# Kernel tuning notes

Hardware: AMD Instinct MI355X
Metric: run time of the kernel (lower is better)

Reference implementation:

```python
import jax, jax.numpy as jnp
import numpy as np

C64 = jnp.complex64


def _apply_1q(state, G, wire):
    # state: [B,2,2,2,2]; G: [2,2] (shared) or [B,2,2] (per-sample)
    s = jnp.moveaxis(state, wire + 1, -1)
    if G.ndim == 2:
        s = jnp.einsum('ij,b...j->b...i', G, s)
    else:
        s = jnp.einsum('bij,b...j->b...i', G, s)
    return jnp.moveaxis(s, -1, wire + 1)


def _apply_cnot(state, c, t):
    s = jnp.moveaxis(state, (c + 1, t + 1), (-2, -1))
    s = jnp.concatenate([s[..., :1, :], s[..., 1:, ::-1]], axis=-2)
    return jnp.moveaxis(s, (-2, -1), (c + 1, t + 1))


def _rx_batch(theta):
    # theta: [B,4] -> gates [B,4,2,2] (PennyLane AngleEmbedding default = RX)
    c = jnp.cos(theta * 0.5).astype(C64)
    s = (-1j * jnp.sin(theta * 0.5)).astype(C64)
    return jnp.stack([jnp.stack([c, s], -1), jnp.stack([s, c], -1)], -2)


def _ry(theta):
    c = jnp.cos(theta * 0.5).astype(C64)
    s = jnp.sin(theta * 0.5).astype(C64)
    return jnp.stack([jnp.stack([c, -s]), jnp.stack([s, c])])


def _rz(theta):
    t = theta.astype(C64)
    return jnp.diag(jnp.stack([jnp.exp(-0.5j * t), jnp.exp(0.5j * t)]))


def _circuit(features, q_params):
    # features: [B,4] angles, q_params: [8]. Returns <Z_w> per wire: [B,4]
    B = features.shape[0]
    state = jnp.zeros((B, 2, 2, 2, 2), C64).at[:, 0, 0, 0, 0].set(1.0)
    Gx = _rx_batch(features)  # [B,4,2,2]
    for w in range(4):
        state = _apply_1q(state, Gx[:, w], w)
    for w in range(4):
        state = _apply_1q(state, _ry(q_params[w]), w)
    for w in range(3):
        state = _apply_cnot(state, w, w + 1)
    for w in range(4):
        state = _apply_1q(state, _rz(q_params[4 + w]), w)
    probs = state.real ** 2 + state.imag ** 2  # [B,2,2,2,2]
    sign = jnp.array([1.0, -1.0], jnp.float32)
    exps = [jnp.sum(probs * sign.reshape([1] + [2 if a == w else 1 for a in range(4)]),
                    axis=(1, 2, 3, 4)) for w in range(4)]
    return jnp.stack(exps, -1)


def setup_inputs() -> dict:
    key = jax.random.key(0)
    ks = jax.random.split(key, 8)
    B = 65536
    return {
        'x': jax.random.normal(ks[0], (B, 1, 36, 36), jnp.float32),
        'q_params': jax.random.normal(ks[1], (8,), jnp.float32),
        'W1': jax.random.normal(ks[2], (64, 4), jnp.float32) * 0.5,
        'b1': jax.random.normal(ks[3], (64,), jnp.float32) * 0.1,
        'W2': jax.random.normal(ks[4], (4, 64), jnp.float32) * 0.125,
        'b2': jax.random.normal(ks[5], (4,), jnp.float32) * 0.1,
        'gamma': jnp.ones((4,), jnp.float32),
        'beta': jnp.zeros((4,), jnp.float32),
    }


def reference(x, q_params, W1, b1, W2, b2, gamma, beta):
    B = x.shape[0]
    # avg_pool2d(kernel=6, stride=6) on [B,1,36,36] -> [B,1,6,6] -> flatten
    pooled = x.reshape(B, 1, 6, 6, 6, 6).mean(axis=(3, 5)).reshape(B, -1)
    features = pooled[:, :4]
    q_out = _circuit(features, q_params)             # [B,4]
    h = jax.nn.relu(q_out @ W1.T + b1)               # [B,64]
    logits = h @ W2.T + b2                           # [B,4]
    # BatchNorm1d (training mode: batch stats, biased var, eps=1e-5)
    mu = logits.mean(axis=0)
    var = ((logits - mu) ** 2).mean(axis=0)
    return gamma * (logits - mu) / jnp.sqrt(var + 1e-5) + beta
```

## Files before the change

### kernel.cpp

```cpp
#include <hip/hip_runtime.h>
#include <math.h>


__global__ void k_init(float* acc) {
    if (threadIdx.x < 8) acc[threadIdx.x] = 0.0f;
}

__global__ __launch_bounds__(256) void k_main(
    const float* __restrict__ x,
    const float* __restrict__ qp,
    const float* __restrict__ W1,
    const float* __restrict__ b1,
    const float* __restrict__ W2,
    const float* __restrict__ b2,
    float* __restrict__ logits,
    float* __restrict__ acc,
    int B)
{
    __shared__ float sW1[256];
    __shared__ float sW2t[256];
    __shared__ float sb1[64];
    __shared__ float sred[32];

    const int tid = threadIdx.x;
    sW1[tid]  = W1[tid];
    sW2t[tid] = W2[(tid & 3) * 64 + (tid >> 2)];
    if (tid < 64) sb1[tid] = b1[tid];
    __syncthreads();

    const int b = blockIdx.x * 256 + tid;
    float l0 = 0.f, l1 = 0.f, l2 = 0.f, l3 = 0.f;

    if (b < B) {
        const float* xb = x + (size_t)b * 1296;
        float f0 = 0.f, f1 = 0.f, f2 = 0.f, f3 = 0.f;
        #pragma unroll
        for (int r = 0; r < 6; ++r) {
            const float4* row = (const float4*)(xb + r * 36);
            float4 v0 = row[0], v1 = row[1], v2 = row[2];
            float4 v3 = row[3], v4 = row[4], v5 = row[5];
            f0 += v0.x + v0.y + v0.z + v0.w + v1.x + v1.y;
            f1 += v1.z + v1.w + v2.x + v2.y + v2.z + v2.w;
            f2 += v3.x + v3.y + v3.z + v3.w + v4.x + v4.y;
            f3 += v4.z + v4.w + v5.x + v5.y + v5.z + v5.w;
        }
        const float inv36 = 1.0f / 36.0f;
        float z0 = cosf(qp[0]) * cosf(f0 * inv36);
        float z1 = cosf(qp[1]) * cosf(f1 * inv36);
        float z2 = cosf(qp[2]) * cosf(f2 * inv36);
        float z3 = cosf(qp[3]) * cosf(f3 * inv36);
        float q0 = z0;
        float q1 = q0 * z1;
        float q2 = q1 * z2;
        float q3 = q2 * z3;

        l0 = b2[0]; l1 = b2[1]; l2 = b2[2]; l3 = b2[3];
        #pragma unroll 8
        for (int j = 0; j < 64; ++j) {
            float h = sb1[j];
            h = fmaf(sW1[4*j+0], q0, h);
            h = fmaf(sW1[4*j+1], q1, h);
            h = fmaf(sW1[4*j+2], q2, h);
            h = fmaxf(fmaf(sW1[4*j+3], q3, h), 0.0f);
            l0 = fmaf(sW2t[4*j+0], h, l0);
            l1 = fmaf(sW2t[4*j+1], h, l1);
            l2 = fmaf(sW2t[4*j+2], h, l2);
            l3 = fmaf(sW2t[4*j+3], h, l3);
        }
        ((float4*)logits)[b] = make_float4(l0, l1, l2, l3);
    }

    float v[8] = {l0, l1, l2, l3, l0*l0, l1*l1, l2*l2, l3*l3};
    #pragma unroll
    for (int off = 32; off >= 1; off >>= 1) {
        #pragma unroll
        for (int i = 0; i < 8; ++i) v[i] += __shfl_down(v[i], off);
    }
    const int lane = tid & 63, wv = tid >> 6;
    if (lane == 0) {
        #pragma unroll
        for (int i = 0; i < 8; ++i) sred[wv * 8 + i] = v[i];
    }
    __syncthreads();
    if (tid < 8) {
        float s = sred[tid] + sred[tid + 8] + sred[tid + 16] + sred[tid + 24];
        atomicAdd(&acc[tid], s);
    }
}

__global__ __launch_bounds__(256) void k_norm(
    const float* __restrict__ logits,
    const float* __restrict__ acc,
    const float* __restrict__ gamma,
    const float* __restrict__ beta,
    float* __restrict__ out,
    int B, float invB)
{
    __shared__ float sc[4], sh[4];
    if (threadIdx.x < 4) {
        const int k = threadIdx.x;
        float mu   = acc[k] * invB;
        float var  = acc[4 + k] * invB - mu * mu;
        float rstd = 1.0f / sqrtf(var + 1e-5f);
        float g = gamma[k] * rstd;
        sc[k] = g;
        sh[k] = beta[k] - mu * g;
    }
    __syncthreads();
    const int b = blockIdx.x * 256 + threadIdx.x;
    if (b >= B) return;
    float4 l = ((const float4*)logits)[b];
    float4 o;
    o.x = fmaf(sc[0], l.x, sh[0]);
    o.y = fmaf(sc[1], l.y, sh[1]);
    o.z = fmaf(sc[2], l.z, sh[2]);
    o.w = fmaf(sc[3], l.w, sh[3]);
    ((float4*)out)[b] = o;
}

extern "C" void kernel_launch(void* const* d_in, const int* in_sizes, int n_in,
                              void* d_out, int out_size, void* d_ws, size_t ws_size,
                              hipStream_t stream) {
    const float* x     = (const float*)d_in[0];
    const float* qp    = (const float*)d_in[1];
    const float* W1    = (const float*)d_in[2];
    const float* b1    = (const float*)d_in[3];
    const float* W2    = (const float*)d_in[4];
    const float* b2    = (const float*)d_in[5];
    const float* gamma = (const float*)d_in[6];
    const float* beta  = (const float*)d_in[7];
    float* out = (float*)d_out;

    const int B = in_sizes[0] / 1296;
    float* acc    = (float*)d_ws;
    float* logits = (float*)d_ws + 64;

    const int nb = (B + 255) / 256;
    hipLaunchKernelGGL(k_init, dim3(1), dim3(64), 0, stream, acc);
    hipLaunchKernelGGL(k_main, dim3(nb), dim3(256), 0, stream,
                       x, qp, W1, b1, W2, b2, logits, acc, B);
    hipLaunchKernelGGL(k_norm, dim3(nb), dim3(256), 0, stream,
                       logits, acc, gamma, beta, out, B, 1.0f / (float)B);
}
```

Measured before the change: 396.9 us.

## Cooperatively load pooled image region with 16 lanes per image

```diff
diff --git a/kernel.cpp b/kernel.cpp
--- a/kernel.cpp
+++ b/kernel.cpp
@@ -5,6 +5,8 @@
 __global__ void k_init(float* acc) {
     if (threadIdx.x < 8) acc[threadIdx.x] = 0.0f;
 }
+
+#define IMGS_PER_BLOCK 64
 
 __global__ __launch_bounds__(256) void k_main(
     const float* __restrict__ x,
@@ -20,35 +22,60 @@
     __shared__ float sW1[256];
     __shared__ float sW2t[256];
     __shared__ float sb1[64];
+    __shared__ float sfeat[IMGS_PER_BLOCK][4];
     __shared__ float sred[32];
 
     const int tid = threadIdx.x;
     sW1[tid]  = W1[tid];
     sW2t[tid] = W2[(tid & 3) * 64 + (tid >> 2)];
     if (tid < 64) sb1[tid] = b1[tid];
+
+    const int g = tid >> 4, l = tid & 15;
+    const int img_base = blockIdx.x * IMGS_PER_BLOCK;
+
+    #pragma unroll
+    for (int r = 0; r < 4; ++r) {
+        const int li  = r * 16 + g;
+        const int img = img_base + li;
+        float f0 = 0.f, f1 = 0.f, f2 = 0.f, f3 = 0.f;
+        if (img < B) {
+            const float* xb = x + (size_t)img * 1296;
+            #pragma unroll
+            for (int k = 0; k < 3; ++k) {
+                const int idx = l + k * 16;
+                if (k == 2 && l >= 4) break;
+                const int row = (idx * 43) >> 8;
+                const int col = idx - 6 * row;
+                float4 v = ((const float4*)(xb + row * 36))[col];
+                float lo = v.x + v.y, hi = v.z + v.w, tot = lo + hi;
+                f0 += (col == 0) ? tot : (col == 1) ? lo : 0.f;
+                f1 += (col == 2) ? tot : (col == 1) ? hi : 0.f;
+                f2 += (col == 3) ? tot : (col == 4) ? lo : 0.f;
+                f3 += (col == 5) ? tot : (col == 4) ? hi : 0.f;
+            }
+        }
+        #pragma unroll
+        for (int m = 1; m < 16; m <<= 1) {
+            f0 += __shfl_xor(f0, m, 16);
+            f1 += __shfl_xor(f1, m, 16);
+            f2 += __shfl_xor(f2, m, 16);
+            f3 += __shfl_xor(f3, m, 16);
+        }
+        if (l == 0) {
+            sfeat[li][0] = f0; sfeat[li][1] = f1;
+            sfeat[li][2] = f2; sfeat[li][3] = f3;
+        }
+    }
     __syncthreads();
 
-    const int b = blockIdx.x * 256 + tid;
     float l0 = 0.f, l1 = 0.f, l2 = 0.f, l3 = 0.f;
-
-    if (b < B) {
-        const float* xb = x + (size_t)b * 1296;
-        float f0 = 0.f, f1 = 0.f, f2 = 0.f, f3 = 0.f;
-        #pragma unroll
-        for (int r = 0; r < 6; ++r) {
-            const float4* row = (const float4*)(xb + r * 36);
-            float4 v0 = row[0], v1 = row[1], v2 = row[2];
-            float4 v3 = row[3], v4 = row[4], v5 = row[5];
-            f0 += v0.x + v0.y + v0.z + v0.w + v1.x + v1.y;
-            f1 += v1.z + v1.w + v2.x + v2.y + v2.z + v2.w;
-            f2 += v3.x + v3.y + v3.z + v3.w + v4.x + v4.y;
-            f3 += v4.z + v4.w + v5.x + v5.y + v5.z + v5.w;
-        }
+    const int img = img_base + tid;
+    if (tid < IMGS_PER_BLOCK && img < B) {
         const float inv36 = 1.0f / 36.0f;
-        float z0 = cosf(qp[0]) * cosf(f0 * inv36);
-        float z1 = cosf(qp[1]) * cosf(f1 * inv36);
-        float z2 = cosf(qp[2]) * cosf(f2 * inv36);
-        float z3 = cosf(qp[3]) * cosf(f3 * inv36);
+        float z0 = cosf(qp[0]) * cosf(sfeat[tid][0] * inv36);
+        float z1 = cosf(qp[1]) * cosf(sfeat[tid][1] * inv36);
+        float z2 = cosf(qp[2]) * cosf(sfeat[tid][2] * inv36);
+        float z3 = cosf(qp[3]) * cosf(sfeat[tid][3] * inv36);
         float q0 = z0;
         float q1 = q0 * z1;
         float q2 = q1 * z2;
@@ -67,7 +94,7 @@
             l2 = fmaf(sW2t[4*j+2], h, l2);
             l3 = fmaf(sW2t[4*j+3], h, l3);
         }
-        ((float4*)logits)[b] = make_float4(l0, l1, l2, l3);
+        ((float4*)logits)[img] = make_float4(l0, l1, l2, l3);
     }
 
     float v[8] = {l0, l1, l2, l3, l0*l0, l1*l1, l2*l2, l3*l3};
@@ -135,10 +162,11 @@
     float* acc    = (float*)d_ws;
     float* logits = (float*)d_ws + 64;
 
-    const int nb = (B + 255) / 256;
+    const int nb_main = (B + IMGS_PER_BLOCK - 1) / IMGS_PER_BLOCK;
+    const int nb_norm = (B + 255) / 256;
     hipLaunchKernelGGL(k_init, dim3(1), dim3(64), 0, stream, acc);
-    hipLaunchKernelGGL(k_main, dim3(nb), dim3(256), 0, stream,
+    hipLaunchKernelGGL(k_main, dim3(nb_main), dim3(256), 0, stream,
                        x, qp, W1, b1, W2, b2, logits, acc, B);
-    hipLaunchKernelGGL(k_norm, dim3(nb), dim3(256), 0, stream,
+    hipLaunchKernelGGL(k_norm, dim3(nb_norm), dim3(256), 0, stream,
                        logits, acc, gamma, beta, out, B, 1.0f / (float)B);
 }
```

New measurement: 406.8 us. +2.5%, slower.
